# Performance work log

Measured on AMD Instinct MI355X. Metric: run time of the kernel, lower is better.

The kernel has to match this reference:

```python
import jax, jax.numpy as jnp
import numpy as np

H = 1024

def setup_inputs() -> dict:
    key = jax.random.key(0)
    ks = jax.random.split(key, 7)
    s = 1.0 / np.sqrt(H)
    return {
        "hidden_states": jax.random.normal(ks[0], (4, 2048, H), dtype=jnp.float32),
        "Wq": jax.random.uniform(ks[1], (H, H), jnp.float32, -s, s),
        "bq": jax.random.uniform(ks[2], (H,), jnp.float32, -s, s),
        "Wk": jax.random.uniform(ks[3], (H, H), jnp.float32, -s, s),
        "bk": jax.random.uniform(ks[4], (H,), jnp.float32, -s, s),
        "Wv": jax.random.uniform(ks[5], (H, H), jnp.float32, -s, s),
        "bv": jax.random.uniform(ks[6], (H,), jnp.float32, -s, s),
    }

def reference(hidden_states, Wq, bq, Wk, bk, Wv, bv):
    # Linear projections (torch Linear: x @ W.T + b)
    q = hidden_states @ Wq.T + bq  # [B,S,H]
    k = hidden_states @ Wk.T + bk
    v = hidden_states @ Wv.T + bv
    # Unscaled attention
    probs = jax.nn.softmax(jnp.einsum("bqh,bkh->bqk", q, k), axis=-1)  # [B,S,S]
    attention_scores = jnp.sum(probs, axis=-2)  # [B,S] column sums
    context = jnp.einsum("bqk,bkh->bqh", probs, v)  # [B,S,H]
    return (context, attention_scores)
```

## Files before the change

### kernel.cpp

```cpp
#include <hip/hip_runtime.h>
#include <stdint.h>


typedef __attribute__((ext_vector_type(8))) short short8;
typedef __attribute__((ext_vector_type(4))) float floatx4;
typedef __attribute__((ext_vector_type(4))) unsigned short ushort4v;
typedef unsigned short u16;

__device__ __forceinline__ u16 f2bf(float f) {
  union { float f; uint32_t u; } v; v.f = f;
  uint32_t u = v.u;
  return (u16)((u + 0x7FFFu + ((u >> 16) & 1u)) >> 16);
}
__device__ __forceinline__ float bf2f(u16 h) {
  union { uint32_t u; float f; } v; v.u = ((uint32_t)h) << 16; return v.f;
}

#define AS3(p) ((__attribute__((address_space(3))) void*)(uint32_t)(uintptr_t)(p))
#define AS1(p) ((__attribute__((address_space(1))) void*)(uintptr_t)(p))

__global__ __launch_bounds__(256) void cvt_all_kernel(
    const float* __restrict__ hs, const float* __restrict__ Wq,
    const float* __restrict__ Wk, const float* __restrict__ Wv,
    u16* __restrict__ hsb, u16* __restrict__ Wb, float* __restrict__ lsum) {
  const int bx = blockIdx.x;
  const float* src;
  u16* dst;
  int i;
  if (bx < 8192) {
    i = bx * 1024 + threadIdx.x * 4;
    src = hs; dst = hsb;
  } else {
    const int idx = bx - 8192;
    const int p = idx >> 10, blk = idx & 1023;
    src = (p == 0) ? Wq : (p == 1) ? Wk : Wv;
    dst = Wb + p * 1048576;
    i = blk * 1024 + threadIdx.x * 4;
  }
  const float4 v = *(const float4*)(src + i);
  ushort4v o;
  o[0] = f2bf(v.x); o[1] = f2bf(v.y); o[2] = f2bf(v.z); o[3] = f2bf(v.w);
  *(ushort4v*)(dst + i) = o;
  if (bx == 0) {
    float4 z = {0.f, 0.f, 0.f, 0.f};
#pragma unroll
    for (int k = 0; k < 8; ++k)
      *(float4*)(lsum + threadIdx.x * 32 + k * 4) = z;
  }
}

__device__ __forceinline__ void gemm_core(const u16* __restrict__ A,
                                          const u16* __restrict__ B,
                                          int lda, int ldb, int K,
                                          u16* As, u16* Bs, floatx4 acc[4][4]) {
  const int tid  = threadIdx.x;
  const int lane = tid & 63;
  const int w    = tid >> 6;
  const int wr   = (w >> 1) * 64;
  const int wc   = (w & 1) * 64;
  const int fr   = lane & 15;
  const int quad = lane >> 4;

  const u16* pa[4];
  const u16* pb[4];
#pragma unroll
  for (int j = 0; j < 4; ++j) {
    const int q   = tid + j * 256;
    const int row = q >> 3, col = q & 7;
    const int gc  = col ^ (row & 7);
    pa[j] = A + row * lda + gc * 8;
    pb[j] = B + row * ldb + gc * 8;
  }

  for (int kk = 0; kk < K; kk += 64) {
#pragma unroll
    for (int j = 0; j < 4; ++j) {
      __builtin_amdgcn_global_load_lds(AS1(pa[j]), AS3(As + (tid + j * 256) * 8), 16, 0, 0);
      __builtin_amdgcn_global_load_lds(AS1(pb[j]), AS3(Bs + (tid + j * 256) * 8), 16, 0, 0);
      pa[j] += 64; pb[j] += 64;
    }
    __syncthreads();
#pragma unroll
    for (int ks = 0; ks < 2; ++ks) {
      const int pc = ((ks * 4 + quad) ^ (fr & 7)) * 8;
      short8 af[4], bfr[4];
#pragma unroll
      for (int i = 0; i < 4; ++i) {
        af[i]  = *(const short8*)(As + (wr + i * 16 + fr) * 64 + pc);
        bfr[i] = *(const short8*)(Bs + (wc + i * 16 + fr) * 64 + pc);
      }
#pragma unroll
      for (int mi = 0; mi < 4; ++mi)
#pragma unroll
        for (int ni = 0; ni < 4; ++ni)
          acc[mi][ni] = __builtin_amdgcn_mfma_f32_16x16x32_bf16(af[mi], bfr[ni],
                                                                acc[mi][ni], 0, 0, 0);
    }
    __syncthreads();
  }
}

__global__ __launch_bounds__(256, 3) void proj_kernel(
    const u16* __restrict__ hsb, const u16* __restrict__ Wb,
    const float* __restrict__ bq, const float* __restrict__ bk,
    const float* __restrict__ bv,
    u16* __restrict__ qo, u16* __restrict__ ko, u16* __restrict__ vt) {
  __shared__ __align__(16) u16 As[8192];
  __shared__ __align__(16) u16 Bs[8192];
  floatx4 acc[4][4];
#pragma unroll
  for (int i = 0; i < 4; ++i)
#pragma unroll
    for (int j = 0; j < 4; ++j) acc[i][j] = {0.f, 0.f, 0.f, 0.f};

  const int p  = blockIdx.z;
  const int m0 = blockIdx.x * 128;
  const int n0 = blockIdx.y * 128;
  gemm_core(hsb + m0 * 1024, Wb + p * 1048576 + n0 * 1024, 1024, 1024, 1024, As, Bs, acc);

  const float* bias = (p == 0) ? bq : (p == 1) ? bk : bv;
  const int lane = threadIdx.x & 63, w = threadIdx.x >> 6;
  const int wr = (w >> 1) * 64, wc = (w & 1) * 64;
  const int col = lane & 15, rg4 = (lane >> 4) * 4;

  if (p < 2) {
    u16* out = (p == 0) ? qo : ko;
#pragma unroll
    for (int mi = 0; mi < 4; ++mi)
#pragma unroll
      for (int ni = 0; ni < 4; ++ni) {
        const int n = n0 + wc + ni * 16 + col;
        const float bn = bias[n];
#pragma unroll
        for (int r = 0; r < 4; ++r) {
          const int m = m0 + wr + mi * 16 + rg4 + r;
          out[m * 1024 + n] = f2bf(acc[mi][ni][r] + bn);
        }
      }
  } else {
#pragma unroll
    for (int mi = 0; mi < 4; ++mi) {
      const int mbase = m0 + wr + mi * 16 + rg4;
      const int b = mbase >> 11, s = mbase & 2047;
#pragma unroll
      for (int ni = 0; ni < 4; ++ni) {
        const int n = n0 + wc + ni * 16 + col;
        const float bn = bias[n];
        ushort4v pk;
#pragma unroll
        for (int r = 0; r < 4; ++r) pk[r] = f2bf(acc[mi][ni][r] + bn);
        *(ushort4v*)(vt + b * 2097152 + n * 2048 + s) = pk;
      }
    }
  }
}

__global__ __launch_bounds__(256) void logits_kernel(
    const u16* __restrict__ q, const u16* __restrict__ k,
    u16* __restrict__ E, float* __restrict__ lsum) {
  __shared__ __align__(16) u16 As[8192];
  __shared__ __align__(16) u16 Bs[8192];
  floatx4 acc[4][4];
#pragma unroll
  for (int i = 0; i < 4; ++i)
#pragma unroll
    for (int j = 0; j < 4; ++j) acc[i][j] = {0.f, 0.f, 0.f, 0.f};

  const int b  = blockIdx.z;
  const int m0 = blockIdx.y * 128;
  const int n0 = blockIdx.x * 128;
  gemm_core(q + (b * 2048 + m0) * 1024, k + (b * 2048 + n0) * 1024,
            1024, 1024, 1024, As, Bs, acc);

  const int lane = threadIdx.x & 63, w = threadIdx.x >> 6;
  const int wr = (w >> 1) * 64, wc = (w & 1) * 64;
  const int col = lane & 15, rg4 = (lane >> 4) * 4;
  u16* Eb = E + b * 4194304;
  float* lb = lsum + b * 2048;

#pragma unroll
  for (int mi = 0; mi < 4; ++mi) {
    floatx4 rs = {0.f, 0.f, 0.f, 0.f};
    const int rbase = m0 + wr + mi * 16 + rg4;
#pragma unroll
    for (int ni = 0; ni < 4; ++ni) {
      const int n = n0 + wc + ni * 16 + col;
#pragma unroll
      for (int r = 0; r < 4; ++r) {
        const float e = __expf(acc[mi][ni][r]);
        rs[r] += e;
        Eb[(rbase + r) * 2048 + n] = f2bf(e);
      }
    }
#pragma unroll
    for (int off = 1; off < 16; off <<= 1) {
      rs[0] += __shfl_xor(rs[0], off, 64);
      rs[1] += __shfl_xor(rs[1], off, 64);
      rs[2] += __shfl_xor(rs[2], off, 64);
      rs[3] += __shfl_xor(rs[3], off, 64);
    }
    if ((lane & 15) == 0) {
#pragma unroll
      for (int r = 0; r < 4; ++r) atomicAdd(&lb[rbase + r], rs[r]);
    }
  }
}

__global__ __launch_bounds__(256, 3) void context_kernel(
    const u16* __restrict__ E, const u16* __restrict__ vt,
    const float* __restrict__ lsum, float* __restrict__ out) {
  __shared__ __align__(16) u16 As[8192];
  __shared__ __align__(16) u16 Bs[8192];
  floatx4 acc[4][4];
#pragma unroll
  for (int i = 0; i < 4; ++i)
#pragma unroll
    for (int j = 0; j < 4; ++j) acc[i][j] = {0.f, 0.f, 0.f, 0.f};

  const int b  = blockIdx.z;
  const int m0 = blockIdx.y * 128;
  const int n0 = blockIdx.x * 128;
  gemm_core(E + b * 4194304 + m0 * 2048, vt + b * 2097152 + n0 * 2048,
            2048, 2048, 2048, As, Bs, acc);

  const int lane = threadIdx.x & 63, w = threadIdx.x >> 6;
  const int wr = (w >> 1) * 64, wc = (w & 1) * 64;
  const int col = lane & 15, rg4 = (lane >> 4) * 4;
  const float* lb = lsum + b * 2048;

#pragma unroll
  for (int mi = 0; mi < 4; ++mi) {
    const int rbase = m0 + wr + mi * 16 + rg4;
    float rinv[4];
#pragma unroll
    for (int r = 0; r < 4; ++r) rinv[r] = 1.0f / lb[rbase + r];
#pragma unroll
    for (int ni = 0; ni < 4; ++ni) {
      const int n = n0 + wc + ni * 16 + col;
#pragma unroll
      for (int r = 0; r < 4; ++r)
        out[(b * 2048 + rbase + r) * 1024 + n] = acc[mi][ni][r] * rinv[r];
    }
  }
}

__global__ __launch_bounds__(256) void colsum_part_kernel(
    const u16* __restrict__ E, const float* __restrict__ lsum,
    float* __restrict__ part) {
  const int b  = blockIdx.x;
  const int g  = blockIdx.y;
  const int q0 = g * 64;
  const int j  = threadIdx.x * 8;
  const u16* Eb = E + b * 4194304;
  const float* lb = lsum + b * 2048;
  float acc[8];
#pragma unroll
  for (int c = 0; c < 8; ++c) acc[c] = 0.f;
  for (int r = 0; r < 64; ++r) {
    const int qi = q0 + r;
    const float rinv = 1.0f / lb[qi];
    const short8 ev = *(const short8*)(Eb + qi * 2048 + j);
#pragma unroll
    for (int c = 0; c < 8; ++c) acc[c] += bf2f((u16)ev[c]) * rinv;
  }
  float* pb = part + (b * 32 + g) * 2048 + j;
#pragma unroll
  for (int c = 0; c < 8; ++c) pb[c] = acc[c];
}

__global__ __launch_bounds__(256) void colsum_reduce_kernel(
    const float* __restrict__ part, float* __restrict__ scores) {
  const int b = blockIdx.x;
  const int j = blockIdx.y * 256 + threadIdx.x;
  const float* pb = part + b * 32 * 2048 + j;
  float s = 0.f;
#pragma unroll
  for (int g = 0; g < 32; ++g) s += pb[g * 2048];
  scores[b * 2048 + j] = s;
}

extern "C" void kernel_launch(void* const* d_in, const int* in_sizes, int n_in,
                              void* d_out, int out_size, void* d_ws, size_t ws_size,
                              hipStream_t stream) {
  const float* hs = (const float*)d_in[0];
  const float* Wq = (const float*)d_in[1];
  const float* bq = (const float*)d_in[2];
  const float* Wk = (const float*)d_in[3];
  const float* bk = (const float*)d_in[4];
  const float* Wv = (const float*)d_in[5];
  const float* bv = (const float*)d_in[6];

  char* ws = (char*)d_ws;
  u16*   qw  = (u16*)(ws);
  u16*   kw  = (u16*)(ws + (16u << 20));
  u16*   vtw = (u16*)(ws + (32u << 20));
  float* lw  = (float*)(ws + (48u << 20));
  float* pw  = (float*)(ws + (48u << 20) + (128u << 10));
  u16*   hsb = (u16*)(ws + (49u << 20));
  u16*   Wb  = (u16*)(ws + (65u << 20));
  u16*   Ew  = (u16*)(ws + (49u << 20));

  float* outc = (float*)d_out;
  float* outs = outc + 8388608;

  cvt_all_kernel<<<11264, 256, 0, stream>>>(hs, Wq, Wk, Wv, hsb, Wb, lw);
  proj_kernel<<<dim3(64, 8, 3), 256, 0, stream>>>(hsb, Wb, bq, bk, bv, qw, kw, vtw);
  logits_kernel<<<dim3(16, 16, 4), 256, 0, stream>>>(qw, kw, Ew, lw);
  context_kernel<<<dim3(8, 16, 4), 256, 0, stream>>>(Ew, vtw, lw, outc);
  colsum_part_kernel<<<dim3(4, 32), 256, 0, stream>>>(Ew, lw, pw);
  colsum_reduce_kernel<<<dim3(4, 8), 256, 0, stream>>>(pw, outs);
}
```

Before: 252.0 us.

## Rewrite logits GEMM with 256x256 tiles and a 4-stage async LDS pipeline

Replaces the 128x128 logits GEMM with a 512-thread kernel computing 256x256 tiles. It uses a 4-slot LDS ring buffer fed by global_load_lds direct copies, a swizzled LDS layout, and a block-index swizzle for L2 locality. Loads are interleaved with MFMA phases under barriers and setprio. The aim is higher data reuse per tile and better latency hiding in the dominant QK^T GEMM. The cost is 128KB of dynamic LDS, only 256 blocks in total, and heavier register pressure from 32 accumulator fragments.

```diff
diff --git a/kernel.cpp b/kernel.cpp
--- a/kernel.cpp
+++ b/kernel.cpp
@@ -155,36 +155,121 @@
   }
 }
 
-__global__ __launch_bounds__(256) void logits_kernel(
+#define LG_SLOT 16384
+
+__global__ __launch_bounds__(512, 2) void logits256_kernel(
     const u16* __restrict__ q, const u16* __restrict__ k,
     u16* __restrict__ E, float* __restrict__ lsum) {
-  __shared__ __align__(16) u16 As[8192];
-  __shared__ __align__(16) u16 Bs[8192];
-  floatx4 acc[4][4];
-#pragma unroll
-  for (int i = 0; i < 4; ++i)
+  extern __shared__ __align__(16) u16 smem[];
+
+  const int tid  = threadIdx.x;
+  const int lane = tid & 63;
+  const int w    = tid >> 6;
+  const int wm   = w >> 2;
+  const int wn   = w & 3;
+  const int fr   = lane & 15;
+  const int quad = lane >> 4;
+  const int pc   = (quad ^ (fr & 3)) * 8;
+
+  const int flat = blockIdx.x + (blockIdx.y << 3) + (blockIdx.z << 6);
+  const int swz  = ((flat & 7) << 5) | (flat >> 3);
+  const int b    = swz >> 6;
+  const int m0   = ((swz >> 3) & 7) << 8;
+  const int n0   = (swz & 7) << 8;
+
+  const u16* Ag = q + (b * 2048 + m0) * 1024;
+  const u16* Bg = k + (b * 2048 + n0) * 1024;
+
+  const u16* pA[2]; const u16* pB[2];
+  uint32_t dA[2], dB[2];
+#pragma unroll
+  for (int j = 0; j < 2; ++j) {
+    const int c   = tid + j * 512;
+    const int row = c >> 2, kc = c & 3;
+    const int gc  = kc ^ (row & 3);
+    pA[j] = Ag + row * 1024 + gc * 8;
+    pB[j] = Bg + row * 1024 + gc * 8;
+    dA[j] = j * 4096 + tid * 8;
+    dB[j] = 8192 + j * 4096 + tid * 8;
+  }
+
+#define LG_STAGE_A(u) do { u16* sb_ = smem + ((u) & 3) * LG_SLOT;                         \
+    __builtin_amdgcn_global_load_lds(AS1(pA[0] + (u) * 32), AS3(sb_ + dA[0]), 16, 0, 0);  \
+    __builtin_amdgcn_global_load_lds(AS1(pA[1] + (u) * 32), AS3(sb_ + dA[1]), 16, 0, 0); } while (0)
+#define LG_STAGE_B(u) do { u16* sb_ = smem + ((u) & 3) * LG_SLOT;                         \
+    __builtin_amdgcn_global_load_lds(AS1(pB[0] + (u) * 32), AS3(sb_ + dB[0]), 16, 0, 0);  \
+    __builtin_amdgcn_global_load_lds(AS1(pB[1] + (u) * 32), AS3(sb_ + dB[1]), 16, 0, 0); } while (0)
+
+  floatx4 acc[8][4];
+#pragma unroll
+  for (int i = 0; i < 8; ++i)
 #pragma unroll
     for (int j = 0; j < 4; ++j) acc[i][j] = {0.f, 0.f, 0.f, 0.f};
 
-  const int b  = blockIdx.z;
-  const int m0 = blockIdx.y * 128;
-  const int n0 = blockIdx.x * 128;
-  gemm_core(q + (b * 2048 + m0) * 1024, k + (b * 2048 + n0) * 1024,
-            1024, 1024, 1024, As, Bs, acc);
-
-  const int lane = threadIdx.x & 63, w = threadIdx.x >> 6;
-  const int wr = (w >> 1) * 64, wc = (w & 1) * 64;
-  const int col = lane & 15, rg4 = (lane >> 4) * 4;
+  LG_STAGE_A(0); LG_STAGE_B(0);
+  LG_STAGE_A(1); LG_STAGE_B(1);
+  LG_STAGE_A(2); LG_STAGE_B(2);
+  asm volatile("s_waitcnt vmcnt(8)" ::: "memory");
+  __builtin_amdgcn_s_barrier();
+
+  const int arow0 = wm * 128 + fr;
+  const int brow0 = wn * 64 + fr;
+
+#pragma unroll 4
+  for (int t = 0; t < 32; ++t) {
+    const u16* sA = smem + (t & 3) * LG_SLOT;
+    const u16* sB = sA + 8192;
+    short8 bf[4], af[4];
+
+#pragma unroll
+    for (int ni = 0; ni < 4; ++ni)
+      bf[ni] = *(const short8*)(sB + (brow0 + ni * 16) * 32 + pc);
+#pragma unroll
+    for (int mi = 0; mi < 4; ++mi)
+      af[mi] = *(const short8*)(sA + (arow0 + mi * 16) * 32 + pc);
+    if (t < 29) LG_STAGE_A(t + 3);
+    __builtin_amdgcn_s_barrier();
+    asm volatile("s_waitcnt lgkmcnt(0)" ::: "memory");
+    __builtin_amdgcn_sched_barrier(0);
+    __builtin_amdgcn_s_setprio(1);
+#pragma unroll
+    for (int mi = 0; mi < 4; ++mi)
+#pragma unroll
+      for (int ni = 0; ni < 4; ++ni)
+        acc[mi][ni] = __builtin_amdgcn_mfma_f32_16x16x32_bf16(af[mi], bf[ni],
+                                                              acc[mi][ni], 0, 0, 0);
+    __builtin_amdgcn_s_setprio(0);
+    __builtin_amdgcn_s_barrier();
+
+#pragma unroll
+    for (int mi = 0; mi < 4; ++mi)
+      af[mi] = *(const short8*)(sA + (arow0 + 64 + mi * 16) * 32 + pc);
+    if (t < 29) LG_STAGE_B(t + 3);
+    asm volatile("s_waitcnt vmcnt(8)" ::: "memory");
+    __builtin_amdgcn_s_barrier();
+    asm volatile("s_waitcnt lgkmcnt(0)" ::: "memory");
+    __builtin_amdgcn_sched_barrier(0);
+    __builtin_amdgcn_s_setprio(1);
+#pragma unroll
+    for (int mi = 0; mi < 4; ++mi)
+#pragma unroll
+      for (int ni = 0; ni < 4; ++ni)
+        acc[mi + 4][ni] = __builtin_amdgcn_mfma_f32_16x16x32_bf16(af[mi], bf[ni],
+                                                                  acc[mi + 4][ni], 0, 0, 0);
+    __builtin_amdgcn_s_setprio(0);
+    __builtin_amdgcn_s_barrier();
+  }
+
   u16* Eb = E + b * 4194304;
   float* lb = lsum + b * 2048;
-
-#pragma unroll
-  for (int mi = 0; mi < 4; ++mi) {
+  const int colw = n0 + wn * 64 + fr;
+#pragma unroll
+  for (int mi = 0; mi < 8; ++mi) {
     floatx4 rs = {0.f, 0.f, 0.f, 0.f};
-    const int rbase = m0 + wr + mi * 16 + rg4;
+    const int rbase = m0 + wm * 128 + mi * 16 + quad * 4;
 #pragma unroll
     for (int ni = 0; ni < 4; ++ni) {
-      const int n = n0 + wc + ni * 16 + col;
+      const int n = colw + ni * 16;
 #pragma unroll
       for (int r = 0; r < 4; ++r) {
         const float e = __expf(acc[mi][ni][r]);
@@ -199,7 +284,7 @@
       rs[2] += __shfl_xor(rs[2], off, 64);
       rs[3] += __shfl_xor(rs[3], off, 64);
     }
-    if ((lane & 15) == 0) {
+    if (fr == 0) {
 #pragma unroll
       for (int r = 0; r < 4; ++r) atomicAdd(&lb[rbase + r], rs[r]);
     }
@@ -303,9 +388,16 @@
   float* outc = (float*)d_out;
   float* outs = outc + 8388608;
 
+  static int s_attr_done = 0;
+  if (!s_attr_done) {
+    (void)hipFuncSetAttribute((const void*)logits256_kernel,
+                              hipFuncAttributeMaxDynamicSharedMemorySize, 131072);
+    s_attr_done = 1;
+  }
+
   cvt_all_kernel<<<11264, 256, 0, stream>>>(hs, Wq, Wk, Wv, hsb, Wb, lw);
   proj_kernel<<<dim3(64, 8, 3), 256, 0, stream>>>(hsb, Wb, bq, bk, bv, qw, kw, vtw);
-  logits_kernel<<<dim3(16, 16, 4), 256, 0, stream>>>(qw, kw, Ew, lw);
+  logits256_kernel<<<dim3(8, 8, 4), 512, 131072, stream>>>(qw, kw, Ew, lw);
   context_kernel<<<dim3(8, 16, 4), 256, 0, stream>>>(Ew, vtw, lw, outc);
   colsum_part_kernel<<<dim3(4, 32), 256, 0, stream>>>(Ew, lw, pw);
   colsum_reduce_kernel<<<dim3(4, 8), 256, 0, stream>>>(pw, outs);
```

After: 250.3 us. Within noise of the previous version (-0.7%).

## Replace GEMM core with triple-buffered 256x128 pipelined core and swizzled grids

Applied to the files above, without the earlier changes.

Replaces the single-buffered 128x128 GEMM core, which used 4 waves and synchronised on every K step, with a templated deep core. The new core uses 8 waves on 256x128 tiles and a 3-slot LDS ring in dynamic shared memory. Global-to-LDS loads for tile t+2 are issued while MFMAs run on tile t, with explicit vmcnt/lgkmcnt waits, split barriers and s_setprio, to hide load latency behind compute. Block indices are swizzled to improve L2 reuse across the projection, logits and context GEMMs. The 144KB of LDS per block limits occupancy to one block per CU.

```diff
diff --git a/kernel.cpp b/kernel.cpp
--- a/kernel.cpp
+++ b/kernel.cpp
@@ -49,79 +49,133 @@
   }
 }
 
-__device__ __forceinline__ void gemm_core(const u16* __restrict__ A,
+#define DC_SLOT 24576
+
+template <int NT>
+__device__ __forceinline__ void deep_core(const u16* __restrict__ A,
                                           const u16* __restrict__ B,
-                                          int lda, int ldb, int K,
-                                          u16* As, u16* Bs, floatx4 acc[4][4]) {
+                                          int lda, int ldb,
+                                          u16* smem, floatx4 acc[4][4]) {
   const int tid  = threadIdx.x;
   const int lane = tid & 63;
   const int w    = tid >> 6;
-  const int wr   = (w >> 1) * 64;
-  const int wc   = (w & 1) * 64;
+  const int wm   = w >> 1;
+  const int wn   = w & 1;
   const int fr   = lane & 15;
   const int quad = lane >> 4;
-
-  const u16* pa[4];
-  const u16* pb[4];
+  const int pc0  = (quad ^ (fr & 7)) * 8;
+  const int pc1  = ((4 + quad) ^ (fr & 7)) * 8;
+
+  const u16* pA[4]; uint32_t dA[4];
 #pragma unroll
   for (int j = 0; j < 4; ++j) {
-    const int q   = tid + j * 256;
-    const int row = q >> 3, col = q & 7;
-    const int gc  = col ^ (row & 7);
-    pa[j] = A + row * lda + gc * 8;
-    pb[j] = B + row * ldb + gc * 8;
-  }
-
-  for (int kk = 0; kk < K; kk += 64) {
-#pragma unroll
-    for (int j = 0; j < 4; ++j) {
-      __builtin_amdgcn_global_load_lds(AS1(pa[j]), AS3(As + (tid + j * 256) * 8), 16, 0, 0);
-      __builtin_amdgcn_global_load_lds(AS1(pb[j]), AS3(Bs + (tid + j * 256) * 8), 16, 0, 0);
-      pa[j] += 64; pb[j] += 64;
-    }
-    __syncthreads();
-#pragma unroll
-    for (int ks = 0; ks < 2; ++ks) {
-      const int pc = ((ks * 4 + quad) ^ (fr & 7)) * 8;
-      short8 af[4], bfr[4];
-#pragma unroll
-      for (int i = 0; i < 4; ++i) {
-        af[i]  = *(const short8*)(As + (wr + i * 16 + fr) * 64 + pc);
-        bfr[i] = *(const short8*)(Bs + (wc + i * 16 + fr) * 64 + pc);
-      }
-#pragma unroll
-      for (int mi = 0; mi < 4; ++mi)
-#pragma unroll
-        for (int ni = 0; ni < 4; ++ni)
-          acc[mi][ni] = __builtin_amdgcn_mfma_f32_16x16x32_bf16(af[mi], bfr[ni],
-                                                                acc[mi][ni], 0, 0, 0);
-    }
-    __syncthreads();
-  }
-}
-
-__global__ __launch_bounds__(256, 3) void proj_kernel(
+    const int c = tid + j * 512, row = c >> 3, kc = c & 7;
+    pA[j] = A + row * lda + (kc ^ (row & 7)) * 8;
+    dA[j] = c * 8;
+  }
+  const u16* pB[2]; uint32_t dB[2];
+#pragma unroll
+  for (int j = 0; j < 2; ++j) {
+    const int c = tid + j * 512, row = c >> 3, kc = c & 7;
+    pB[j] = B + row * ldb + (kc ^ (row & 7)) * 8;
+    dB[j] = 16384 + c * 8;
+  }
+
+#define DC_STA(u) do { u16* s_ = smem + ((u) % 3) * DC_SLOT;                                  \
+    _Pragma("unroll") for (int j_ = 0; j_ < 4; ++j_)                                           \
+      __builtin_amdgcn_global_load_lds(AS1(pA[j_] + (u) * 64), AS3(s_ + dA[j_]), 16, 0, 0);   \
+  } while (0)
+#define DC_STB(u) do { u16* s_ = smem + ((u) % 3) * DC_SLOT;                                  \
+    _Pragma("unroll") for (int j_ = 0; j_ < 2; ++j_)                                           \
+      __builtin_amdgcn_global_load_lds(AS1(pB[j_] + (u) * 64), AS3(s_ + dB[j_]), 16, 0, 0);   \
+  } while (0)
+
+  DC_STA(0); DC_STB(0); DC_STA(1); DC_STB(1);
+  asm volatile("s_waitcnt vmcnt(6)" ::: "memory");
+  __builtin_amdgcn_s_barrier();
+
+  const int arow0 = wm * 64 + fr;
+  const int brow0 = wn * 64 + fr;
+
+#pragma unroll
+  for (int t = 0; t < NT; ++t) {
+    const u16* sA = smem + (t % 3) * DC_SLOT;
+    const u16* sB = sA + 16384;
+    short8 af[4], bf[4];
+
+#pragma unroll
+    for (int mi = 0; mi < 4; ++mi)
+      af[mi] = *(const short8*)(sA + (arow0 + mi * 16) * 64 + pc0);
+#pragma unroll
+    for (int ni = 0; ni < 4; ++ni)
+      bf[ni] = *(const short8*)(sB + (brow0 + ni * 16) * 64 + pc0);
+    if (t < NT - 2) DC_STA(t + 2);
+    __builtin_amdgcn_s_barrier();
+    asm volatile("s_waitcnt lgkmcnt(0)" ::: "memory");
+    __builtin_amdgcn_sched_barrier(0);
+    __builtin_amdgcn_s_setprio(1);
+#pragma unroll
+    for (int mi = 0; mi < 4; ++mi)
+#pragma unroll
+      for (int ni = 0; ni < 4; ++ni)
+        acc[mi][ni] = __builtin_amdgcn_mfma_f32_16x16x32_bf16(af[mi], bf[ni],
+                                                              acc[mi][ni], 0, 0, 0);
+    __builtin_amdgcn_s_setprio(0);
+    __builtin_amdgcn_s_barrier();
+
+#pragma unroll
+    for (int mi = 0; mi < 4; ++mi)
+      af[mi] = *(const short8*)(sA + (arow0 + mi * 16) * 64 + pc1);
+#pragma unroll
+    for (int ni = 0; ni < 4; ++ni)
+      bf[ni] = *(const short8*)(sB + (brow0 + ni * 16) * 64 + pc1);
+    if (t < NT - 2) {
+      DC_STB(t + 2);
+      asm volatile("s_waitcnt vmcnt(6)" ::: "memory");
+    } else {
+      asm volatile("s_waitcnt vmcnt(0)" ::: "memory");
+    }
+    __builtin_amdgcn_s_barrier();
+    asm volatile("s_waitcnt lgkmcnt(0)" ::: "memory");
+    __builtin_amdgcn_sched_barrier(0);
+    __builtin_amdgcn_s_setprio(1);
+#pragma unroll
+    for (int mi = 0; mi < 4; ++mi)
+#pragma unroll
+      for (int ni = 0; ni < 4; ++ni)
+        acc[mi][ni] = __builtin_amdgcn_mfma_f32_16x16x32_bf16(af[mi], bf[ni],
+                                                              acc[mi][ni], 0, 0, 0);
+    __builtin_amdgcn_s_setprio(0);
+    __builtin_amdgcn_s_barrier();
+  }
+#undef DC_STA
+#undef DC_STB
+}
+
+__global__ __launch_bounds__(512, 2) void proj_deep_kernel(
     const u16* __restrict__ hsb, const u16* __restrict__ Wb,
     const float* __restrict__ bq, const float* __restrict__ bk,
     const float* __restrict__ bv,
     u16* __restrict__ qo, u16* __restrict__ ko, u16* __restrict__ vt) {
-  __shared__ __align__(16) u16 As[8192];
-  __shared__ __align__(16) u16 Bs[8192];
+  extern __shared__ __align__(16) u16 smem[];
   floatx4 acc[4][4];
 #pragma unroll
   for (int i = 0; i < 4; ++i)
 #pragma unroll
     for (int j = 0; j < 4; ++j) acc[i][j] = {0.f, 0.f, 0.f, 0.f};
 
-  const int p  = blockIdx.z;
-  const int m0 = blockIdx.x * 128;
-  const int n0 = blockIdx.y * 128;
-  gemm_core(hsb + m0 * 1024, Wb + p * 1048576 + n0 * 1024, 1024, 1024, 1024, As, Bs, acc);
+  const int p    = blockIdx.z;
+  const int flat = blockIdx.x + blockIdx.y * 8;
+  const int swz  = (flat & 7) * 32 + (flat >> 3);
+  const int m0   = (swz >> 3) * 256;
+  const int n0   = (swz & 7) * 128;
+
+  deep_core<16>(hsb + m0 * 1024, Wb + p * 1048576 + n0 * 1024, 1024, 1024, smem, acc);
 
   const float* bias = (p == 0) ? bq : (p == 1) ? bk : bv;
   const int lane = threadIdx.x & 63, w = threadIdx.x >> 6;
-  const int wr = (w >> 1) * 64, wc = (w & 1) * 64;
-  const int col = lane & 15, rg4 = (lane >> 4) * 4;
+  const int wm = w >> 1, wn = w & 1;
+  const int fr = lane & 15, rg4 = (lane >> 4) * 4;
 
   if (p < 2) {
     u16* out = (p == 0) ? qo : ko;
@@ -129,22 +183,22 @@
     for (int mi = 0; mi < 4; ++mi)
 #pragma unroll
       for (int ni = 0; ni < 4; ++ni) {
-        const int n = n0 + wc + ni * 16 + col;
+        const int n = n0 + wn * 64 + ni * 16 + fr;
         const float bn = bias[n];
 #pragma unroll
         for (int r = 0; r < 4; ++r) {
-          const int m = m0 + wr + mi * 16 + rg4 + r;
+          const int m = m0 + wm * 64 + mi * 16 + rg4 + r;
           out[m * 1024 + n] = f2bf(acc[mi][ni][r] + bn);
         }
       }
   } else {
 #pragma unroll
     for (int mi = 0; mi < 4; ++mi) {
-      const int mbase = m0 + wr + mi * 16 + rg4;
+      const int mbase = m0 + wm * 64 + mi * 16 + rg4;
       const int b = mbase >> 11, s = mbase & 2047;
 #pragma unroll
       for (int ni = 0; ni < 4; ++ni) {
-        const int n = n0 + wc + ni * 16 + col;
+        const int n = n0 + wn * 64 + ni * 16 + fr;
         const float bn = bias[n];
         ushort4v pk;
 #pragma unroll
@@ -155,36 +209,38 @@
   }
 }
 
-__global__ __launch_bounds__(256) void logits_kernel(
+__global__ __launch_bounds__(512, 2) void logits_deep_kernel(
     const u16* __restrict__ q, const u16* __restrict__ k,
     u16* __restrict__ E, float* __restrict__ lsum) {
-  __shared__ __align__(16) u16 As[8192];
-  __shared__ __align__(16) u16 Bs[8192];
+  extern __shared__ __align__(16) u16 smem[];
   floatx4 acc[4][4];
 #pragma unroll
   for (int i = 0; i < 4; ++i)
 #pragma unroll
     for (int j = 0; j < 4; ++j) acc[i][j] = {0.f, 0.f, 0.f, 0.f};
 
-  const int b  = blockIdx.z;
-  const int m0 = blockIdx.y * 128;
-  const int n0 = blockIdx.x * 128;
-  gemm_core(q + (b * 2048 + m0) * 1024, k + (b * 2048 + n0) * 1024,
-            1024, 1024, 1024, As, Bs, acc);
+  const int flat = blockIdx.x + blockIdx.y * 16 + blockIdx.z * 128;
+  const int swz  = (flat & 7) * 64 + (flat >> 3);
+  const int b    = swz >> 7;
+  const int m0   = ((swz >> 4) & 7) * 256;
+  const int n0   = (swz & 15) * 128;
+
+  deep_core<16>(q + (b * 2048 + m0) * 1024, k + (b * 2048 + n0) * 1024,
+                1024, 1024, smem, acc);
 
   const int lane = threadIdx.x & 63, w = threadIdx.x >> 6;
-  const int wr = (w >> 1) * 64, wc = (w & 1) * 64;
-  const int col = lane & 15, rg4 = (lane >> 4) * 4;
+  const int wm = w >> 1, wn = w & 1;
+  const int fr = lane & 15, quad = lane >> 4;
   u16* Eb = E + b * 4194304;
   float* lb = lsum + b * 2048;
 
 #pragma unroll
   for (int mi = 0; mi < 4; ++mi) {
     floatx4 rs = {0.f, 0.f, 0.f, 0.f};
-    const int rbase = m0 + wr + mi * 16 + rg4;
+    const int rbase = m0 + wm * 64 + mi * 16 + quad * 4;
 #pragma unroll
     for (int ni = 0; ni < 4; ++ni) {
-      const int n = n0 + wc + ni * 16 + col;
+      const int n = n0 + wn * 64 + ni * 16 + fr;
 #pragma unroll
       for (int r = 0; r < 4; ++r) {
         const float e = __expf(acc[mi][ni][r]);
@@ -199,44 +255,46 @@
       rs[2] += __shfl_xor(rs[2], off, 64);
       rs[3] += __shfl_xor(rs[3], off, 64);
     }
-    if ((lane & 15) == 0) {
+    if (fr == 0) {
 #pragma unroll
       for (int r = 0; r < 4; ++r) atomicAdd(&lb[rbase + r], rs[r]);
     }
   }
 }
 
-__global__ __launch_bounds__(256, 3) void context_kernel(
+__global__ __launch_bounds__(512, 2) void context_deep_kernel(
     const u16* __restrict__ E, const u16* __restrict__ vt,
     const float* __restrict__ lsum, float* __restrict__ out) {
-  __shared__ __align__(16) u16 As[8192];
-  __shared__ __align__(16) u16 Bs[8192];
+  extern __shared__ __align__(16) u16 smem[];
   floatx4 acc[4][4];
 #pragma unroll
   for (int i = 0; i < 4; ++i)
 #pragma unroll
     for (int j = 0; j < 4; ++j) acc[i][j] = {0.f, 0.f, 0.f, 0.f};
 
-  const int b  = blockIdx.z;
-  const int m0 = blockIdx.y * 128;
-  const int n0 = blockIdx.x * 128;
-  gemm_core(E + b * 4194304 + m0 * 2048, vt + b * 2097152 + n0 * 2048,
-            2048, 2048, 2048, As, Bs, acc);
+  const int flat = blockIdx.x + blockIdx.y * 8 + blockIdx.z * 64;
+  const int swz  = (flat & 7) * 32 + (flat >> 3);
+  const int b    = swz >> 6;
+  const int m0   = ((swz >> 3) & 7) * 256;
+  const int n0   = (swz & 7) * 128;
+
+  deep_core<32>(E + b * 4194304 + m0 * 2048, vt + b * 2097152 + n0 * 2048,
+                2048, 2048, smem, acc);
 
   const int lane = threadIdx.x & 63, w = threadIdx.x >> 6;
-  const int wr = (w >> 1) * 64, wc = (w & 1) * 64;
-  const int col = lane & 15, rg4 = (lane >> 4) * 4;
+  const int wm = w >> 1, wn = w & 1;
+  const int fr = lane & 15, rg4 = (lane >> 4) * 4;
   const float* lb = lsum + b * 2048;
 
 #pragma unroll
   for (int mi = 0; mi < 4; ++mi) {
-    const int rbase = m0 + wr + mi * 16 + rg4;
+    const int rbase = m0 + wm * 64 + mi * 16 + rg4;
     float rinv[4];
 #pragma unroll
     for (int r = 0; r < 4; ++r) rinv[r] = 1.0f / lb[rbase + r];
 #pragma unroll
     for (int ni = 0; ni < 4; ++ni) {
-      const int n = n0 + wc + ni * 16 + col;
+      const int n = n0 + wn * 64 + ni * 16 + fr;
 #pragma unroll
       for (int r = 0; r < 4; ++r)
         out[(b * 2048 + rbase + r) * 1024 + n] = acc[mi][ni][r] * rinv[r];
@@ -303,10 +361,21 @@
   float* outc = (float*)d_out;
   float* outs = outc + 8388608;
 
+  static int s_attr_done = 0;
+  if (!s_attr_done) {
+    (void)hipFuncSetAttribute((const void*)proj_deep_kernel,
+                              hipFuncAttributeMaxDynamicSharedMemorySize, 147456);
+    (void)hipFuncSetAttribute((const void*)logits_deep_kernel,
+                              hipFuncAttributeMaxDynamicSharedMemorySize, 147456);
+    (void)hipFuncSetAttribute((const void*)context_deep_kernel,
+                              hipFuncAttributeMaxDynamicSharedMemorySize, 147456);
+    s_attr_done = 1;
+  }
+
   cvt_all_kernel<<<11264, 256, 0, stream>>>(hs, Wq, Wk, Wv, hsb, Wb, lw);
-  proj_kernel<<<dim3(64, 8, 3), 256, 0, stream>>>(hsb, Wb, bq, bk, bv, qw, kw, vtw);
-  logits_kernel<<<dim3(16, 16, 4), 256, 0, stream>>>(qw, kw, Ew, lw);
-  context_kernel<<<dim3(8, 16, 4), 256, 0, stream>>>(Ew, vtw, lw, outc);
+  proj_deep_kernel<<<dim3(8, 32, 3), 512, 147456, stream>>>(hsb, Wb, bq, bk, bv, qw, kw, vtw);
+  logits_deep_kernel<<<dim3(16, 8, 4), 512, 147456, stream>>>(qw, kw, Ew, lw);
+  context_deep_kernel<<<dim3(8, 8, 4), 512, 147456, stream>>>(Ew, vtw, lw, outc);
   colsum_part_kernel<<<dim3(4, 32), 256, 0, stream>>>(Ew, lw, pw);
   colsum_reduce_kernel<<<dim3(4, 8), 256, 0, stream>>>(pw, outs);
 }
```

Result: faster. 241.4 us (-4.2%).
